# Optimization experiments

Measured on AMD Instinct MI355X. Metric: run time of the kernel, lower is better.

The kernel has to match this reference:

```python
import jax, jax.numpy as jnp
import numpy as np

B, S, D, H = 2, 2048, 1024, 16
DH = D // H
EPS = 1e-5
LAMBDA_INIT = 0.8


def setup_inputs() -> dict:
    key = jax.random.key(0)
    ks = jax.random.split(key, 16)
    w_std = 1.0 / np.sqrt(D)
    lam_std = LAMBDA_INIT / np.sqrt(DH)
    return {
        "x": jax.random.normal(ks[0], (B, S, D), jnp.float32),
        # Linear weights stored [in, out] (y = x @ W + b), equivalent to torch W.T
        "Wq": jax.random.normal(ks[1], (D, D), jnp.float32) * w_std,
        "bq": jax.random.normal(ks[2], (D,), jnp.float32) * 0.02,
        "Wk": jax.random.normal(ks[3], (D, D), jnp.float32) * w_std,
        "bk": jax.random.normal(ks[4], (D,), jnp.float32) * 0.02,
        "Wv": jax.random.normal(ks[5], (D, D), jnp.float32) * w_std,
        "bv": jax.random.normal(ks[6], (D,), jnp.float32) * 0.02,
        "Wo": jax.random.normal(ks[7], (D, D), jnp.float32) * w_std,
        "bo": jax.random.normal(ks[8], (D,), jnp.float32) * 0.02,
        "lq1": jax.random.normal(ks[9], (H, DH), jnp.float32) * lam_std,
        "lk1": jax.random.normal(ks[10], (H, DH), jnp.float32) * lam_std,
        "lq2": jax.random.normal(ks[11], (H, DH), jnp.float32) * lam_std,
        "lk2": jax.random.normal(ks[12], (H, DH), jnp.float32) * lam_std,
        # per-head GroupNorm(1, head_dim) affine params (torch default init)
        "gn_w": jnp.ones((H, DH), jnp.float32),
        "gn_b": jnp.zeros((H, DH), jnp.float32),
    }


def reference(x, Wq, bq, Wk, bk, Wv, bv, Wo, bo, lq1, lk1, lq2, lk2, gn_w, gn_b):
    b, s, d = x.shape
    h, dh = lq1.shape
    scale = dh ** -0.5

    q = (x @ Wq + bq).reshape(b, s, h, dh)
    k = (x @ Wk + bk).reshape(b, s, h, dh)
    v = (x @ Wv + bv).reshape(b, s, h, dh)

    # differential lambda per head: exp(<lq1,lk1>) - exp(<lq2,lk2>) + lambda_init
    lam = jnp.exp((lq1 * lk1).sum(-1)) - jnp.exp((lq2 * lk2).sum(-1)) + LAMBDA_INIT  # [H]

    scores = jnp.einsum("bihd,bjhd->bhij", q, k) * scale * lam[None, :, None, None]
    attn = jax.nn.softmax(scores, axis=-1)  # no mask in default call path
    out = jnp.einsum("bhij,bjhd->bihd", attn, v)  # [B,S,H,DH]

    # per-head GroupNorm(1, head_dim): normalize over (seq, head_dim) per (batch, head)
    mean = out.mean(axis=(1, 3), keepdims=True)
    var = out.var(axis=(1, 3), keepdims=True)
    normed = (out - mean) * jax.lax.rsqrt(var + EPS)
    normed = normed * gn_w[None, None, :, :] + gn_b[None, None, :, :]

    y = normed.reshape(b, s, d) @ Wo + bo
    return y
```

## Files before the change

kernel.cpp:

```cpp
#include <hip/hip_runtime.h>

#define S_LEN 2048
#define D_DIM 1024
#define H_NUM 16
#define DH 64
#define EPS_GN 1e-5f
#define LAMBDA_INIT 0.8f

typedef unsigned short bfu;
typedef __attribute__((ext_vector_type(8))) short bf16x8;
typedef __attribute__((ext_vector_type(4))) float f32x4;

union FragU { uint4 u; bf16x8 f; };

__device__ inline float bf2f(bfu u){
  union { unsigned int i; float f; } c; c.i = ((unsigned int)u) << 16; return c.f;
}
__device__ inline bfu f2bf(float f){
  union { float f; unsigned int u; } c; c.f = f;
  unsigned int r = c.u + 0x7fffu + ((c.u >> 16) & 1u);
  return (bfu)(r >> 16);
}
__device__ inline unsigned cvtpk(float lo, float hi){
  unsigned r;
  asm("v_cvt_pk_bf16_f32 %0, %1, %2" : "=v"(r) : "v"(lo), "v"(hi));
  return r;
}
__device__ inline void gload16(const void* g, void* lds){
  __builtin_amdgcn_global_load_lds(
      (const __attribute__((address_space(1))) void*)g,
      (__attribute__((address_space(3))) void*)lds, 16, 0, 0);
}
__device__ inline float ldx(const void* p, size_t i, int isf32){
  return isf32 ? ((const float*)p)[i] : bf2f(((const bfu*)p)[i]);
}
__device__ inline float wave_sum(float x){
  #pragma unroll
  for (int off = 32; off; off >>= 1) x += __shfl_xor(x, off, 64);
  return x;
}

__global__ void lambda_kernel(const void* __restrict__ lq1, const void* __restrict__ lk1,
                              const void* __restrict__ lq2, const void* __restrict__ lk2,
                              const unsigned int* __restrict__ gnw_bits,
                              int* __restrict__ flag, float* __restrict__ lam,
                              float* __restrict__ sums){
  const int isf32 = (gnw_bits[0] == 0x3F800000u) ? 1 : 0;
  int t = threadIdx.x;
  if (t == 0) flag[0] = isf32;
  sums[t] = 0.f;
  if (t < H_NUM){
    float s1 = 0.f, s2 = 0.f;
    for (int d = 0; d < DH; ++d){
      s1 += ldx(lq1, t*DH+d, isf32) * ldx(lk1, t*DH+d, isf32);
      s2 += ldx(lq2, t*DH+d, isf32) * ldx(lk2, t*DH+d, isf32);
    }
    lam[t] = expf(s1) - expf(s2) + LAMBDA_INIT;
  }
}

__global__ __launch_bounds__(256) void prep_all(
    const void* __restrict__ x,
    const void* __restrict__ w0, const void* __restrict__ w1,
    const void* __restrict__ w2, const void* __restrict__ w3,
    const int* __restrict__ flag, bfu* __restrict__ xb, bfu* __restrict__ wt)
{
  const int isf32 = flag[0];
  if (blockIdx.x < 2048){
    size_t i = ((size_t)blockIdx.x * 256 + threadIdx.x) * 8;
    if (isf32){
      const float* xf = (const float*)x;
      float4 a = *(const float4*)(xf + i);
      float4 b = *(const float4*)(xf + i + 4);
      bfu o[8] = {f2bf(a.x),f2bf(a.y),f2bf(a.z),f2bf(a.w),f2bf(b.x),f2bf(b.y),f2bf(b.z),f2bf(b.w)};
      *(uint4*)(xb + i) = *(const uint4*)o;
    } else {
      *(uint4*)(xb + i) = *(const uint4*)((const bfu*)x + i);
    }
    return;
  }
  const int widx = blockIdx.x - 2048;
  const int wsel = widx >> 8, tile = widx & 255;
  const void* W = (wsel==0)?w0:(wsel==1)?w1:(wsel==2)?w2:w3;
  bfu* dst = wt + (size_t)wsel * D_DIM * D_DIM;
  __shared__ float Ts[64][65];
  const int r0 = (tile >> 4) * 64, c0 = (tile & 15) * 64;
  const int ty = threadIdx.x >> 6, tx = threadIdx.x & 63;
  #pragma unroll
  for (int rr = 0; rr < 16; ++rr){
    int row = ty*16 + rr;
    Ts[row][tx] = ldx(W, (size_t)(r0 + row) * D_DIM + c0 + tx, isf32);
  }
  __syncthreads();
  #pragma unroll
  for (int rr = 0; rr < 16; ++rr){
    int row = ty*16 + rr;
    dst[(size_t)(c0 + row) * D_DIM + r0 + tx] = f2bf(Ts[tx][row]);
  }
}

__global__ __launch_bounds__(256, 3) void qkv_mfma(
    const bfu* __restrict__ xb, const bfu* __restrict__ wt,
    const void* __restrict__ bq, const void* __restrict__ bk, const void* __restrict__ bv,
    const float* __restrict__ lam, const int* __restrict__ flag,
    bfu* __restrict__ qb, bfu* __restrict__ kb, bfu* __restrict__ vt)
{
  const int isf32 = flag[0];
  const int z = blockIdx.z;
  const bfu* Wt = wt + (size_t)z * D_DIM * D_DIM;
  const void* bias = (z==0)?bq:(z==1)?bk:bv;

  __shared__ __align__(16) ushort As[2][128][32];
  __shared__ __align__(16) ushort Bs[2][128][32];
  const int m0 = blockIdx.x * 128, n0 = blockIdx.y * 128;
  const int t = threadIdx.x, w = t >> 6, lane = t & 63;
  const int quad = lane >> 4, l15 = lane & 15;
  const int mbase = (w >> 1) * 64, nbase = (w & 1) * 64;

  const int srow = w*32 + (lane >> 2);
  const int gchunk = (lane & 3) ^ ((lane >> 3) & 3);
  const size_t aoff = (size_t)(m0 + srow) * D_DIM + gchunk*8;
  const size_t boff = (size_t)(n0 + srow) * D_DIM + gchunk*8;

#define STAGE(buf, k0) {                                                  \
    gload16(xb + aoff + (k0),            &As[buf][w*32][0]);              \
    gload16(xb + aoff + 16*D_DIM + (k0), &As[buf][w*32+16][0]);           \
    gload16(Wt + boff + (k0),            &Bs[buf][w*32][0]);              \
    gload16(Wt + boff + 16*D_DIM + (k0), &Bs[buf][w*32+16][0]);           \
  }

  f32x4 acc[4][4];
  #pragma unroll
  for (int i = 0; i < 4; ++i)
    #pragma unroll
    for (int j = 0; j < 4; ++j){ f32x4 zz = {0.f,0.f,0.f,0.f}; acc[i][j] = zz; }

  const int chq = (quad ^ ((l15 >> 1) & 3)) * 8;

  STAGE(0, 0)
  int buf = 0;
  for (int k0 = 0; k0 < D_DIM; k0 += 32){
    if (k0 + 32 < D_DIM){
      STAGE(buf ^ 1, k0 + 32)
      asm volatile("s_waitcnt vmcnt(4)" ::: "memory");
    } else {
      asm volatile("s_waitcnt vmcnt(0)" ::: "memory");
    }
    __builtin_amdgcn_s_barrier();
    FragU af[4], bf[4];
    #pragma unroll
    for (int mt = 0; mt < 4; ++mt) af[mt].u = *(const uint4*)&As[buf][mbase + mt*16 + l15][chq];
    #pragma unroll
    for (int nt = 0; nt < 4; ++nt) bf[nt].u = *(const uint4*)&Bs[buf][nbase + nt*16 + l15][chq];
    #pragma unroll
    for (int mt = 0; mt < 4; ++mt)
      #pragma unroll
      for (int nt = 0; nt < 4; ++nt)
        acc[mt][nt] = __builtin_amdgcn_mfma_f32_16x16x32_bf16(af[mt].f, bf[nt].f, acc[mt][nt], 0, 0, 0);
    __builtin_amdgcn_s_barrier();
    buf ^= 1;
  }
#undef STAGE

  #pragma unroll
  for (int mt = 0; mt < 4; ++mt){
    const int mrow = m0 + mbase + mt*16 + quad*4;
    #pragma unroll
    for (int nt = 0; nt < 4; ++nt){
      const int n = n0 + nbase + nt*16 + l15;
      const float bn = ldx(bias, n, isf32);
      if (z < 2){
        bfu* out = (z == 0) ? qb : kb;
        const float qs = (z == 0) ? 0.18033688f * lam[n >> 6] : 1.0f;
        #pragma unroll
        for (int r = 0; r < 4; ++r)
          out[(size_t)(mrow + r) * D_DIM + n] = f2bf((acc[mt][nt][r] + bn) * qs);
      } else {
        const int b = mrow >> 11, s = mrow & (S_LEN - 1);
        const int h = n >> 6, d = n & 63;
        ushort4 pk;
        pk.x = f2bf(acc[mt][nt][0] + bn); pk.y = f2bf(acc[mt][nt][1] + bn);
        pk.z = f2bf(acc[mt][nt][2] + bn); pk.w = f2bf(acc[mt][nt][3] + bn);
        *(ushort4*)(vt + (((size_t)(b*H_NUM + h)*DH + d)*S_LEN) + s) = pk;
      }
    }
  }
}

__global__ __launch_bounds__(256) void repack_k(const bfu* __restrict__ kb, bfu* __restrict__ ksw){
  __shared__ __align__(16) ushort L[64][72];
  const int b = blockIdx.z, h = blockIdx.y, j0 = blockIdx.x * 64;
  const int t = threadIdx.x;
  const int bh = b*H_NUM + h;
  {
    const int j = t >> 2, seg = (t & 3) * 16;
    const bfu* src = kb + ((size_t)(b*S_LEN + j0 + j)*H_NUM + h)*DH + seg;
    uint4 a = *(const uint4*)src, c = *(const uint4*)(src + 8);
    *(uint4*)&L[j][seg] = a; *(uint4*)&L[j][seg+8] = c;
  }
  __syncthreads();
  #pragma unroll
  for (int half = 0; half < 2; ++half){
    int c16 = half*256 + t;
    int blk = c16 >> 6;
    int l   = c16 & 63;
    int jt = blk >> 1, c = blk & 1;
    int m = l & 15, q = l >> 4;
    uint4 v = *(const uint4*)&L[jt*16 + m][c*32 + q*8];
    bfu* dst = ksw + (((size_t)bh*128 + (j0>>4) + jt)*2 + c)*512 + (size_t)l*8;
    *(uint4*)dst = v;
  }
}

__global__ __launch_bounds__(256) void repack_v(const bfu* __restrict__ vt, bfu* __restrict__ vsw){
  __shared__ __align__(16) ushort L[64][72];
  const int b = blockIdx.z, h = blockIdx.y, j0 = blockIdx.x * 64;
  const int t = threadIdx.x;
  const int bh = b*H_NUM + h;
  {
    const int d = t >> 2, seg = (t & 3) * 16;
    const bfu* src = vt + ((size_t)bh*DH + d)*S_LEN + j0 + seg;
    uint4 a = *(const uint4*)src, c = *(const uint4*)(src + 8);
    *(uint4*)&L[d][seg] = a; *(uint4*)&L[d][seg+8] = c;
  }
  __syncthreads();
  #pragma unroll
  for (int half = 0; half < 2; ++half){
    int c16 = half*256 + t;
    int blk = c16 >> 6;
    int l   = c16 & 63;
    int dt = blk >> 1, jcl = blk & 1;
    int m = l & 15, q = l >> 4;
    const int jb = jcl*32 + 16*(q>>1) + 4*(q&1);
    uint2 v0 = *(const uint2*)&L[dt*16 + m][jb];
    uint2 v1 = *(const uint2*)&L[dt*16 + m][jb + 8];
    uint4 v; v.x = v0.x; v.y = v0.y; v.z = v1.x; v.w = v1.y;
    bfu* dst = vsw + (((size_t)bh*4 + dt)*64 + (j0>>5) + jcl)*512 + (size_t)l*8;
    *(uint4*)dst = v;
  }
}

__global__ __launch_bounds__(256, 2) void attn_mfma(
    const bfu* __restrict__ qb, const bfu* __restrict__ ksw, const bfu* __restrict__ vsw,
    bfu* __restrict__ o)
{
  const int b = blockIdx.z, h = blockIdx.y, i0 = blockIdx.x * 128;
  const int t = threadIdx.x, w = t >> 6, lane = t & 63;
  const int quad = lane >> 4, l15 = lane & 15;
  const int bh = b*H_NUM + h;

  FragU qf[2][2];
  #pragma unroll
  for (int mt = 0; mt < 2; ++mt){
    const bfu* qrow = qb + ((size_t)(b*S_LEN + i0 + w*32 + mt*16 + l15)*H_NUM + h)*DH;
    qf[mt][0].u = *(const uint4*)(qrow + quad*8);
    qf[mt][1].u = *(const uint4*)(qrow + 32 + quad*8);
  }

  const bfu* kbase = ksw + (size_t)bh*131072 + (size_t)lane*8;
  const bfu* vbase = vsw + (size_t)bh*131072 + (size_t)lane*8;

  f32x4 Oacc[2][4];
  #pragma unroll
  for (int mt = 0; mt < 2; ++mt)
    #pragma unroll
    for (int dt = 0; dt < 4; ++dt){ f32x4 zz = {0.f,0.f,0.f,0.f}; Oacc[mt][dt] = zz; }
  float lsum[2] = {0.f, 0.f};

  FragU kfA[4][2], vfA[2][4], kfB[4][2], vfB[2][4];

#define LOAD_K(KF, J0)                                                          \
  { _Pragma("unroll")                                                           \
    for (int jt = 0; jt < 4; ++jt){                                             \
      const bfu* kr = kbase + (size_t)(((J0)>>4) + jt)*1024;                    \
      KF[jt][0].u = *(const uint4*)kr;                                          \
      KF[jt][1].u = *(const uint4*)(kr + 512);                                  \
    } }
#define LOAD_V(VF, J0)                                                          \
  { _Pragma("unroll")                                                           \
    for (int jt2 = 0; jt2 < 2; ++jt2)                                           \
      _Pragma("unroll")                                                         \
      for (int dt = 0; dt < 4; ++dt)                                            \
        VF[jt2][dt].u = *(const uint4*)(vbase + (size_t)(dt*64 + ((J0)>>5) + jt2)*512); }

#define PROCESS(KF, VF)                                                         \
  {                                                                             \
    f32x4 s[2][4];                                                              \
    _Pragma("unroll")                                                           \
    for (int jt = 0; jt < 4; ++jt){                                             \
      _Pragma("unroll")                                                         \
      for (int mt = 0; mt < 2; ++mt){                                           \
        f32x4 zz = {0.f,0.f,0.f,0.f};                                           \
        zz = __builtin_amdgcn_mfma_f32_16x16x32_bf16(KF[jt][0].f, qf[mt][0].f, zz, 0, 0, 0); \
        zz = __builtin_amdgcn_mfma_f32_16x16x32_bf16(KF[jt][1].f, qf[mt][1].f, zz, 0, 0, 0); \
        s[mt][jt] = zz;                                                         \
      }                                                                         \
    }                                                                           \
    _Pragma("unroll")                                                           \
    for (int mt = 0; mt < 2; ++mt){                                             \
      float ps = 0.f;                                                           \
      _Pragma("unroll")                                                         \
      for (int jt = 0; jt < 4; ++jt){                                           \
        _Pragma("unroll")                                                       \
        for (int r = 0; r < 4; ++r){                                            \
          float p = __builtin_exp2f(s[mt][jt][r]);                              \
          s[mt][jt][r] = p;                                                     \
          ps += p;                                                              \
        }                                                                       \
      }                                                                         \
      lsum[mt] += ps;                                                           \
      _Pragma("unroll")                                                         \
      for (int jt2 = 0; jt2 < 2; ++jt2){                                        \
        unsigned pa0 = cvtpk(s[mt][2*jt2][0],   s[mt][2*jt2][1]);               \
        unsigned pa1 = cvtpk(s[mt][2*jt2][2],   s[mt][2*jt2][3]);               \
        unsigned pb0 = cvtpk(s[mt][2*jt2+1][0], s[mt][2*jt2+1][1]);             \
        unsigned pb1 = cvtpk(s[mt][2*jt2+1][2], s[mt][2*jt2+1][3]);             \
        auto r0 = __builtin_amdgcn_permlane32_swap(pa0, pb0, false, false);     \
        auto r1 = __builtin_amdgcn_permlane32_swap(pa1, pb1, false, false);     \
        FragU pf;                                                               \
        pf.u.x = r0[0]; pf.u.y = r1[0]; pf.u.z = r0[1]; pf.u.w = r1[1];         \
        _Pragma("unroll")                                                       \
        for (int dt = 0; dt < 4; ++dt)                                          \
          Oacc[mt][dt] = __builtin_amdgcn_mfma_f32_16x16x32_bf16(VF[jt2][dt].f, pf.f, Oacc[mt][dt], 0, 0, 0); \
      }                                                                         \
    }                                                                           \
  }

  LOAD_K(kfA, 0)
  LOAD_V(vfA, 0)
  for (int j0 = 0; j0 < S_LEN; j0 += 128){
    LOAD_K(kfB, j0 + 64)
    LOAD_V(vfB, j0 + 64)
    PROCESS(kfA, vfA)
    if (j0 + 128 < S_LEN){
      LOAD_K(kfA, j0 + 128)
      LOAD_V(vfA, j0 + 128)
    }
    PROCESS(kfB, vfB)
  }
#undef LOAD_K
#undef LOAD_V
#undef PROCESS

  #pragma unroll
  for (int mt = 0; mt < 2; ++mt){
    float l = lsum[mt];
    l += __shfl_xor(l, 16, 64);
    l += __shfl_xor(l, 32, 64);
    float inv = 1.f / l;
    bfu* orow = o + ((size_t)(b*S_LEN + i0 + w*32 + mt*16 + l15)*H_NUM + h)*DH;
    #pragma unroll
    for (int dt = 0; dt < 4; ++dt){
      ushort4 pk;
      pk.x = f2bf(Oacc[mt][dt][0]*inv); pk.y = f2bf(Oacc[mt][dt][1]*inv);
      pk.z = f2bf(Oacc[mt][dt][2]*inv); pk.w = f2bf(Oacc[mt][dt][3]*inv);
      *(ushort4*)(orow + dt*16 + quad*4) = pk;
    }
  }
}

__global__ __launch_bounds__(256) void gn_part(const bfu* __restrict__ o, float* __restrict__ sums){
  const int bh = blockIdx.x >> 3, chunk = blockIdx.x & 7;
  const int b = bh >> 4, h = bh & 15;
  const bfu* base = o + ((size_t)(b*S_LEN + chunk*256)*H_NUM + h)*DH;
  float s1 = 0.f, s2 = 0.f;
  for (int u = threadIdx.x*4; u < 256*64; u += 256*4){
    int s = u >> 6, d = u & 63;
    ushort4 p = *(const ushort4*)(base + (size_t)s * D_DIM + d);
    float v0 = bf2f(p.x), v1 = bf2f(p.y), v2 = bf2f(p.z), v3 = bf2f(p.w);
    s1 += v0+v1+v2+v3; s2 += v0*v0+v1*v1+v2*v2+v3*v3;
  }
  s1 = wave_sum(s1); s2 = wave_sum(s2);
  __shared__ float r1[4], r2[4];
  int w = threadIdx.x >> 6, lane = threadIdx.x & 63;
  if (lane == 0){ r1[w] = s1; r2[w] = s2; }
  __syncthreads();
  if (threadIdx.x == 0){
    atomicAdd(&sums[bh*2+0], r1[0]+r1[1]+r1[2]+r1[3]);
    atomicAdd(&sums[bh*2+1], r2[0]+r2[1]+r2[2]+r2[3]);
  }
}

__global__ __launch_bounds__(256) void gn_fold(
    const bfu* __restrict__ wt,
    const void* __restrict__ bo, const float* __restrict__ sums,
    const void* __restrict__ gnw, const void* __restrict__ gnb,
    const int* __restrict__ flag,
    bfu* __restrict__ wt2, float* __restrict__ beta)
{
  const int isf32 = flag[0];
  const int z = blockIdx.y;
  const int t = threadIdx.x;
  const int n = blockIdx.x*16 + (t >> 4);
  const int seg = t & 15;
  const float invN = 1.f / (float)(S_LEN * DH);
  const float s1 = sums[(z*H_NUM + seg)*2], s2 = sums[(z*H_NUM + seg)*2 + 1];
  const float mu = s1 * invN;
  const float ri = rsqrtf(s2 * invN - mu*mu + EPS_GN);
  const bfu* src = wt + (size_t)n * D_DIM + seg*64;
  bfu* dst = wt2 + (size_t)z * D_DIM * D_DIM + (size_t)n * D_DIM + seg*64;
  float bacc = 0.f;
  #pragma unroll
  for (int i0 = 0; i0 < 64; i0 += 8){
    uint4 wv = *(const uint4*)(src + i0);
    const bfu* wp = (const bfu*)&wv;
    bfu outv[8];
    #pragma unroll
    for (int j = 0; j < 8; ++j){
      const int c = seg*64 + i0 + j;
      const float wq = bf2f(wp[j]);
      const float a = ri * ldx(gnw, c, isf32);
      outv[j] = f2bf(wq * a);
      bacc += (ldx(gnb, c, isf32) - mu * a) * wq;
    }
    *(uint4*)(dst + i0) = *(const uint4*)outv;
  }
  #pragma unroll
  for (int off = 1; off < 16; off <<= 1) bacc += __shfl_xor(bacc, off, 64);
  if (seg == 0) beta[z*D_DIM + n] = bacc + ldx(bo, n, isf32);
}

__global__ __launch_bounds__(256) void oproj_mfma(
    const bfu* __restrict__ ob, const bfu* __restrict__ wt2,
    const float* __restrict__ beta, const int* __restrict__ flag, void* __restrict__ y)
{
  const int isf32 = flag[0];
  __shared__ __align__(16) ushort As[64][40];
  __shared__ __align__(16) ushort Bs[128][40];
  const int m0 = blockIdx.x * 64, n0 = blockIdx.y * 128;
  const int t = threadIdx.x, w = t >> 6, lane = t & 63;
  const int quad = lane >> 4, l15 = lane & 15;
  const int mbase = (w >> 1) * 32, nbase = (w & 1) * 64;
  const int bB = m0 >> 11;
  const bfu* Wt = wt2 + (size_t)bB * D_DIM * D_DIM;
  const float* bet = beta + bB * D_DIM;

  const int arow = t >> 2, aseg = (t & 3) * 8;
  const int brow = t >> 1, bhalf = (t & 1) * 16;

  f32x4 acc[2][4];
  #pragma unroll
  for (int i = 0; i < 2; ++i)
    #pragma unroll
    for (int j = 0; j < 4; ++j){ f32x4 zz = {0.f,0.f,0.f,0.f}; acc[i][j] = zz; }

  for (int k0 = 0; k0 < D_DIM; k0 += 32){
    *(uint4*)&As[arow][aseg] = *(const uint4*)(ob + (size_t)(m0 + arow) * D_DIM + k0 + aseg);
    const bfu* bsrc = Wt + (size_t)(n0 + brow) * D_DIM + k0 + bhalf;
    uint4 b0 = *(const uint4*)bsrc, b1 = *(const uint4*)(bsrc + 8);
    *(uint4*)&Bs[brow][bhalf]     = b0;  *(uint4*)&Bs[brow][bhalf + 8] = b1;
    __syncthreads();
    FragU af[2], bfr[4];
    #pragma unroll
    for (int mt = 0; mt < 2; ++mt) af[mt].u = *(const uint4*)&As[mbase + mt*16 + l15][quad*8];
    #pragma unroll
    for (int nt = 0; nt < 4; ++nt) bfr[nt].u = *(const uint4*)&Bs[nbase + nt*16 + l15][quad*8];
    #pragma unroll
    for (int mt = 0; mt < 2; ++mt)
      #pragma unroll
      for (int nt = 0; nt < 4; ++nt)
        acc[mt][nt] = __builtin_amdgcn_mfma_f32_16x16x32_bf16(af[mt].f, bfr[nt].f, acc[mt][nt], 0, 0, 0);
    __syncthreads();
  }

  #pragma unroll
  for (int mt = 0; mt < 2; ++mt){
    const int mrow = m0 + mbase + mt*16 + quad*4;
    #pragma unroll
    for (int nt = 0; nt < 4; ++nt){
      const int n = n0 + nbase + nt*16 + l15;
      const float bn = bet[n];
      #pragma unroll
      for (int r = 0; r < 4; ++r){
        float val = acc[mt][nt][r] + bn;
        if (isf32) ((float*)y)[(size_t)(mrow + r) * D_DIM + n] = val;
        else       ((bfu*)y)[(size_t)(mrow + r) * D_DIM + n] = f2bf(val);
      }
    }
  }
}

extern "C" void kernel_launch(void* const* d_in, const int* in_sizes, int n_in,
                              void* d_out, int out_size, void* d_ws, size_t ws_size,
                              hipStream_t stream)
{
  const void* x   = d_in[0];
  const void* Wq  = d_in[1];
  const void* bq  = d_in[2];
  const void* Wk  = d_in[3];
  const void* bk  = d_in[4];
  const void* Wv  = d_in[5];
  const void* bv  = d_in[6];
  const void* Wo  = d_in[7];
  const void* bo  = d_in[8];
  const void* lq1 = d_in[9];
  const void* lk1 = d_in[10];
  const void* lq2 = d_in[11];
  const void* lk2 = d_in[12];
  const void* gnw = d_in[13];
  const void* gnb = d_in[14];

  float* ws   = (float*)d_ws;
  int*   flag = (int*)d_ws;
  float* lam  = ws + 16;
  float* sums = ws + 48;

  const size_t MB = 1u << 20;
  char* base = (char*)d_ws + 4096;
  bfu* xb  = (bfu*)(base);
  bfu* wt  = (bfu*)(base + 8*MB);
  bfu* qb  = (bfu*)(base + 16*MB);
  bfu* kb  = (bfu*)(base + 24*MB);
  bfu* vt  = (bfu*)(base + 32*MB);
  bfu* ob  = (bfu*)(base + 40*MB);
  bfu* ksw = xb;
  bfu* vsw = kb;
  bfu* wt2 = vt;
  float* beta = (float*)(base + 36*MB);

  lambda_kernel<<<1, 64, 0, stream>>>(lq1, lk1, lq2, lk2, (const unsigned int*)gnw, flag, lam, sums);
  prep_all<<<3072, 256, 0, stream>>>(x, Wq, Wk, Wv, Wo, flag, xb, wt);
  qkv_mfma<<<dim3(32, 8, 3), 256, 0, stream>>>(xb, wt, bq, bk, bv, lam, flag, qb, kb, vt);
  repack_k<<<dim3(32, 16, 2), 256, 0, stream>>>(kb, ksw);
  repack_v<<<dim3(32, 16, 2), 256, 0, stream>>>(vt, vsw);
  attn_mfma<<<dim3(16, 16, 2), 256, 0, stream>>>(qb, ksw, vsw, ob);
  gn_part<<<256, 256, 0, stream>>>(ob, sums);
  gn_fold<<<dim3(64, 2), 256, 0, stream>>>(wt + (size_t)3*D_DIM*D_DIM, bo, sums, gnw, gnb, flag, wt2, beta);
  oproj_mfma<<<dim3(64, 8), 256, 0, stream>>>(ob, wt2, beta, flag, d_out);
}
```

Measured before the change: 271.4 us.

## Fuse GroupNorm statistics into attention epilogue, swizzle workgroups, add MFMA priority

```diff
diff --git a/kernel.cpp b/kernel.cpp
--- a/kernel.cpp
+++ b/kernel.cpp
@@ -242,12 +242,16 @@
 
 __global__ __launch_bounds__(256, 2) void attn_mfma(
     const bfu* __restrict__ qb, const bfu* __restrict__ ksw, const bfu* __restrict__ vsw,
-    bfu* __restrict__ o)
+    bfu* __restrict__ o, float* __restrict__ sums)
 {
-  const int b = blockIdx.z, h = blockIdx.y, i0 = blockIdx.x * 128;
+  const int wg = blockIdx.x;
+  const int swz = (wg & 7) * 64 + (wg >> 3);
+  const int g = swz >> 4;
+  const int i0 = (swz & 15) * 128;
+  const int h = g & 15, b = g >> 4;
   const int t = threadIdx.x, w = t >> 6, lane = t & 63;
   const int quad = lane >> 4, l15 = lane & 15;
-  const int bh = b*H_NUM + h;
+  const int bh = g;
 
   FragU qf[2][2];
   #pragma unroll
@@ -286,6 +290,7 @@
 #define PROCESS(KF, VF)                                                         \
   {                                                                             \
     f32x4 s[2][4];                                                              \
+    __builtin_amdgcn_s_setprio(1);                                              \
     _Pragma("unroll")                                                           \
     for (int jt = 0; jt < 4; ++jt){                                             \
       _Pragma("unroll")                                                         \
@@ -296,6 +301,7 @@
         s[mt][jt] = zz;                                                         \
       }                                                                         \
     }                                                                           \
+    __builtin_amdgcn_s_setprio(0);                                              \
     _Pragma("unroll")                                                           \
     for (int mt = 0; mt < 2; ++mt){                                             \
       float ps = 0.f;                                                           \
@@ -319,9 +325,11 @@
         auto r1 = __builtin_amdgcn_permlane32_swap(pa1, pb1, false, false);     \
         FragU pf;                                                               \
         pf.u.x = r0[0]; pf.u.y = r1[0]; pf.u.z = r0[1]; pf.u.w = r1[1];         \
+        __builtin_amdgcn_s_setprio(1);                                          \
         _Pragma("unroll")                                                       \
         for (int dt = 0; dt < 4; ++dt)                                          \
           Oacc[mt][dt] = __builtin_amdgcn_mfma_f32_16x16x32_bf16(VF[jt2][dt].f, pf.f, Oacc[mt][dt], 0, 0, 0); \
+        __builtin_amdgcn_s_setprio(0);                                          \
       }                                                                         \
     }                                                                           \
   }
@@ -342,6 +350,7 @@
 #undef LOAD_V
 #undef PROCESS
 
+  float s1 = 0.f, s2 = 0.f;
   #pragma unroll
   for (int mt = 0; mt < 2; ++mt){
     float l = lsum[mt];
@@ -351,31 +360,20 @@
     bfu* orow = o + ((size_t)(b*S_LEN + i0 + w*32 + mt*16 + l15)*H_NUM + h)*DH;
     #pragma unroll
     for (int dt = 0; dt < 4; ++dt){
+      float v0 = Oacc[mt][dt][0]*inv, v1 = Oacc[mt][dt][1]*inv;
+      float v2 = Oacc[mt][dt][2]*inv, v3 = Oacc[mt][dt][3]*inv;
+      s1 += (v0+v1) + (v2+v3);
+      s2 += (v0*v0+v1*v1) + (v2*v2+v3*v3);
       ushort4 pk;
-      pk.x = f2bf(Oacc[mt][dt][0]*inv); pk.y = f2bf(Oacc[mt][dt][1]*inv);
-      pk.z = f2bf(Oacc[mt][dt][2]*inv); pk.w = f2bf(Oacc[mt][dt][3]*inv);
+      pk.x = f2bf(v0); pk.y = f2bf(v1); pk.z = f2bf(v2); pk.w = f2bf(v3);
       *(ushort4*)(orow + dt*16 + quad*4) = pk;
     }
-  }
-}
-
-__global__ __launch_bounds__(256) void gn_part(const bfu* __restrict__ o, float* __restrict__ sums){
-  const int bh = blockIdx.x >> 3, chunk = blockIdx.x & 7;
-  const int b = bh >> 4, h = bh & 15;
-  const bfu* base = o + ((size_t)(b*S_LEN + chunk*256)*H_NUM + h)*DH;
-  float s1 = 0.f, s2 = 0.f;
-  for (int u = threadIdx.x*4; u < 256*64; u += 256*4){
-    int s = u >> 6, d = u & 63;
-    ushort4 p = *(const ushort4*)(base + (size_t)s * D_DIM + d);
-    float v0 = bf2f(p.x), v1 = bf2f(p.y), v2 = bf2f(p.z), v3 = bf2f(p.w);
-    s1 += v0+v1+v2+v3; s2 += v0*v0+v1*v1+v2*v2+v3*v3;
   }
   s1 = wave_sum(s1); s2 = wave_sum(s2);
   __shared__ float r1[4], r2[4];
-  int w = threadIdx.x >> 6, lane = threadIdx.x & 63;
   if (lane == 0){ r1[w] = s1; r2[w] = s2; }
   __syncthreads();
-  if (threadIdx.x == 0){
+  if (t == 0){
     atomicAdd(&sums[bh*2+0], r1[0]+r1[1]+r1[2]+r1[3]);
     atomicAdd(&sums[bh*2+1], r2[0]+r2[1]+r2[2]+r2[3]);
   }
@@ -523,8 +521,7 @@
   qkv_mfma<<<dim3(32, 8, 3), 256, 0, stream>>>(xb, wt, bq, bk, bv, lam, flag, qb, kb, vt);
   repack_k<<<dim3(32, 16, 2), 256, 0, stream>>>(kb, ksw);
   repack_v<<<dim3(32, 16, 2), 256, 0, stream>>>(vt, vsw);
-  attn_mfma<<<dim3(16, 16, 2), 256, 0, stream>>>(qb, ksw, vsw, ob);
-  gn_part<<<256, 256, 0, stream>>>(ob, sums);
+  attn_mfma<<<512, 256, 0, stream>>>(qb, ksw, vsw, ob, sums);
   gn_fold<<<dim3(64, 2), 256, 0, stream>>>(wt + (size_t)3*D_DIM*D_DIM, bo, sums, gnw, gnb, flag, wt2, beta);
   oproj_mfma<<<dim3(64, 8), 256, 0, stream>>>(ob, wt2, beta, flag, d_out);
 }
```

New measurement: 262.4 us. -3.3%, faster.
